# Performance work log

Hardware: AMD Instinct MI355X
Metric: run time of the kernel (lower is better)

## Reference

```python
import jax, jax.numpy as jnp
import numpy as np

N_NODES = 50000
N_EDGES = 800000
IN_FEATS = 32
OUT_FEATS = 32
NUM_HEADS = 4


def setup_inputs() -> dict:
    key = jax.random.key(0)
    ks = jax.random.split(key, 12)
    H, F, IN = NUM_HEADS, OUT_FEATS, IN_FEATS
    h = jax.random.normal(ks[0], (N_NODES, IN), dtype=jnp.float32)
    src = jax.random.randint(ks[1], (N_EDGES,), 0, N_NODES, dtype=jnp.int64)
    dst = jax.random.randint(ks[2], (N_EDGES,), 0, N_NODES, dtype=jnp.int64)
    s = 0.1
    W_gat = jax.random.normal(ks[3], (IN, H * F), dtype=jnp.float32) * s
    attn_l = jax.random.normal(ks[4], (H, F), dtype=jnp.float32) * s
    attn_r = jax.random.normal(ks[5], (H, F), dtype=jnp.float32) * s
    W_ih = jax.random.normal(ks[6], (3 * F, H * F), dtype=jnp.float32) * s
    W_hh = jax.random.normal(ks[7], (3 * F, F), dtype=jnp.float32) * s
    b_ih = jax.random.normal(ks[8], (3 * F,), dtype=jnp.float32) * s
    b_hh = jax.random.normal(ks[9], (3 * F,), dtype=jnp.float32) * s
    return {"h": h, "W_gat": W_gat, "attn_l": attn_l, "attn_r": attn_r,
            "W_ih": W_ih, "W_hh": W_hh, "b_ih": b_ih, "b_hh": b_hh,
            "src": src, "dst": dst}


def reference(h, W_gat, attn_l, attn_r, W_ih, W_hh, b_ih, b_hh, src, dst):
    N = h.shape[0]
    H, F = attn_l.shape
    # --- GATConv ---
    feat = (h @ W_gat).reshape(N, H, F)                      # (N,H,F)
    el = jnp.einsum('nhf,hf->nh', feat, attn_l)              # (N,H)
    er = jnp.einsum('nhf,hf->nh', feat, attn_r)              # (N,H)
    e = jax.nn.leaky_relu(el[src] + er[dst], 0.2)            # (E,H) edge logits
    emax = jax.ops.segment_max(e, dst, num_segments=N)       # per-dst max (stable)
    ee = jnp.exp(e - emax[dst])
    denom = jax.ops.segment_sum(ee, dst, num_segments=N)
    alpha = ee / denom[dst]                                  # segment softmax (E,H)
    msg = feat[src] * alpha[:, :, None]                      # (E,H,F)
    agg = jax.ops.segment_sum(msg, dst, num_segments=N)      # (N,H,F)
    x = agg.reshape(N, H * F)
    # --- GRUCell (torch semantics, gate order r,z,n) ---
    gi = x @ W_ih.T + b_ih                                   # (N,3F)
    gh = h @ W_hh.T + b_hh                                   # (N,3F)
    i_r, i_z, i_n = jnp.split(gi, 3, axis=1)
    h_r, h_z, h_n = jnp.split(gh, 3, axis=1)
    r = jax.nn.sigmoid(i_r + h_r)
    z = jax.nn.sigmoid(i_z + h_z)
    n = jnp.tanh(i_n + r * h_n)
    h_new = (1.0 - z) * n + z * h
    return jax.nn.elu(h_new)
```

## Files before the change

kernel.cpp:

```cpp
#include <hip/hip_runtime.h>
#include <hip/hip_bf16.h>
#include <cmath>

#define N_NODES 50000
#define N_EDGES 800000
#define CAP 64

#define NBINS 196
#define BIN_CAP 8192
#define CUR_PAD 32

#define P1_EPT 2
#define P1_EPB (1024 * P1_EPT)
#define P1_BLOCKS ((N_EDGES + P1_EPB - 1) / P1_EPB)

#define HB_BLOCKS 98
#define ELR_BLOCKS 196
#define WC_BLOCKS 30
#define NB_HB  (P1_BLOCKS)
#define NB_ELR (NB_HB + HB_BLOCKS)
#define NB_WC  (NB_ELR + ELR_BLOCKS)
#define NB_WGB (NB_WC + WC_BLOCKS)
#define PREP_TOTAL (NB_WGB + 1)

#define AGGR_BLOCKS (N_NODES / 16)

typedef __attribute__((ext_vector_type(8))) short bf16x8;
typedef __attribute__((ext_vector_type(4))) float f32x4;

__device__ inline short bfbits(float x) {
    __hip_bfloat16 t = __float2bfloat16(x);
    return *reinterpret_cast<short*>(&t);
}
__device__ inline unsigned short bfu16(float x) {
    __hip_bfloat16 t = __float2bfloat16(x);
    return *reinterpret_cast<unsigned short*>(&t);
}

__global__ __launch_bounds__(1024) void k_part_prep(
        const int* __restrict__ src, const int* __restrict__ dst,
        int* __restrict__ bin_cursor, unsigned* __restrict__ bin_buf,
        const float* __restrict__ h, const float* __restrict__ Wg,
        const float* __restrict__ al, const float* __restrict__ ar,
        const float* __restrict__ Wih, const float* __restrict__ Whh,
        unsigned short* __restrict__ hb, float* __restrict__ el,
        float* __restrict__ er, __hip_bfloat16* __restrict__ Wc,
        __hip_bfloat16* __restrict__ Wgb) {
    const int t = threadIdx.x;
    __shared__ union {
        struct {
            int bcnt[256], bofs[256], cur[256], gbase[256];
            int wt4[4];
            unsigned stage[P1_EPB];
        } part;
        __hip_bfloat16 vlr[16][32];
    } sm;

    if (blockIdx.x < P1_BLOCKS) {
        int* bcnt = sm.part.bcnt; int* bofs = sm.part.bofs;
        int* cur = sm.part.cur;   int* gbase = sm.part.gbase;
        int* wt4 = sm.part.wt4;   unsigned* stage = sm.part.stage;
        if (t < 256) bcnt[t] = 0;
        __syncthreads();
        int bn0 = -1, bn1 = -1;
        unsigned pk0 = 0, pk1 = 0;
        const int ebase = blockIdx.x * P1_EPB + t * 2;
        if (ebase < N_EDGES) {
            const int2 dd = *(const int2*)(dst + ebase);
            const int2 ss = *(const int2*)(src + ebase);
            bn0 = dd.x >> 8; pk0 = (unsigned)ss.x | ((unsigned)dd.x << 16);
            bn1 = dd.y >> 8; pk1 = (unsigned)ss.y | ((unsigned)dd.y << 16);
            atomicAdd(&bcnt[bn0], 1);
            atomicAdd(&bcnt[bn1], 1);
        }
        __syncthreads();
        int x = 0, vv = 0;
        if (t < 256) {
            vv = bcnt[t];
            x = vv;
            const int lane = t & 63;
#pragma unroll
            for (int m = 1; m < 64; m <<= 1) {
                const int y = __shfl_up(x, m, 64);
                if (lane >= m) x += y;
            }
            if (lane == 63) wt4[t >> 6] = x;
        }
        __syncthreads();
        if (t < 256) {
            const int wave4 = t >> 6;
            int wb = 0;
#pragma unroll
            for (int i = 0; i < 4; ++i) if (i < wave4) wb += wt4[i];
            const int off = wb + x - vv;
            bofs[t] = off;
            cur[t] = off;
            gbase[t] = (vv > 0) ? atomicAdd(&bin_cursor[t * CUR_PAD], vv) : 0;
        }
        __syncthreads();
        if (bn0 >= 0) {
            stage[atomicAdd(&cur[bn0], 1)] = pk0;
            stage[atomicAdd(&cur[bn1], 1)] = pk1;
        }
        __syncthreads();
        const int tot = wt4[0] + wt4[1] + wt4[2] + wt4[3];
        for (int i = t; i < tot; i += 1024) {
            const unsigned e = stage[i];
            const int b = e >> 24;
            const int gi = gbase[b] + (i - bofs[b]);
            if (gi < BIN_CAP) bin_buf[(size_t)b * BIN_CAP + gi] = e;
        }
        return;
    }
    if (blockIdx.x < NB_ELR) {
        const int idx = (blockIdx.x - NB_HB) * 1024 + t;
        const int base = idx * 16;
        if (base < N_NODES * 32) {
            const float4* hp = (const float4*)(h + base);
            const float4 v0 = hp[0], v1 = hp[1], v2 = hp[2], v3 = hp[3];
            unsigned o[8];
            o[0] = (unsigned)bfu16(v0.x) | ((unsigned)bfu16(v0.y) << 16);
            o[1] = (unsigned)bfu16(v0.z) | ((unsigned)bfu16(v0.w) << 16);
            o[2] = (unsigned)bfu16(v1.x) | ((unsigned)bfu16(v1.y) << 16);
            o[3] = (unsigned)bfu16(v1.z) | ((unsigned)bfu16(v1.w) << 16);
            o[4] = (unsigned)bfu16(v2.x) | ((unsigned)bfu16(v2.y) << 16);
            o[5] = (unsigned)bfu16(v2.z) | ((unsigned)bfu16(v2.w) << 16);
            o[6] = (unsigned)bfu16(v3.x) | ((unsigned)bfu16(v3.y) << 16);
            o[7] = (unsigned)bfu16(v3.z) | ((unsigned)bfu16(v3.w) << 16);
            uint4* op = (uint4*)(hb + base);
            op[0] = (uint4){o[0], o[1], o[2], o[3]};
            op[1] = (uint4){o[4], o[5], o[6], o[7]};
        }
        return;
    }
    if (blockIdx.x < NB_WC) {
        if (t < 512) {
            const int col = t >> 5, k = t & 31;
            float v = 0.f;
            if (col < 8) {
                const int hd = col & 3;
                const float* a = (col < 4) ? (al + hd * 32) : (ar + hd * 32);
                const float* w = Wg + k * 128 + hd * 32;
#pragma unroll
                for (int f = 0; f < 32; ++f) v = fmaf(w[f], a[f], v);
            }
            sm.vlr[col][k] = __float2bfloat16(v);
        }
        __syncthreads();
        const int wave = t >> 6, lane = t & 63;
        const int li = lane & 15, quad = lane >> 4;
        const int mt = (blockIdx.x - NB_ELR) * 16 + wave;
        if (mt >= AGGR_BLOCKS) return;
        const int m_base = mt * 16;
        bf16x8 a;
        {
            const float4* hp = (const float4*)(h + (size_t)(m_base + li) * 32 + quad * 8);
            const float4 f0 = hp[0], f1 = hp[1];
            a[0] = bfbits(f0.x); a[1] = bfbits(f0.y); a[2] = bfbits(f0.z); a[3] = bfbits(f0.w);
            a[4] = bfbits(f1.x); a[5] = bfbits(f1.y); a[6] = bfbits(f1.z); a[7] = bfbits(f1.w);
        }
        const bf16x8 b = *(const bf16x8*)(&sm.vlr[li][0] + quad * 8);
        f32x4 acc = (f32x4){0.f, 0.f, 0.f, 0.f};
        acc = __builtin_amdgcn_mfma_f32_16x16x32_bf16(a, b, acc, 0, 0, 0);
        if (li < 8) {
#pragma unroll
            for (int i = 0; i < 4; ++i) {
                const int m = m_base + quad * 4 + i;
                if (li < 4) el[m * 4 + li] = acc[i];
                else        er[m * 4 + (li - 4)] = acc[i];
            }
        }
        return;
    }
    if (blockIdx.x < NB_WGB) {
        const int idx = (blockIdx.x - NB_WC) * 1024 + t;
        const int r = idx / 160, k = idx - r * 160;
        float v = 0.f;
        if (r < 96) { if (k < 128) v = Wih[r * 128 + k]; }
        else        { if (k >= 128) v = Whh[(r - 96) * 32 + (k - 128)]; }
        Wc[idx] = __float2bfloat16(v);
        return;
    }
#pragma unroll
    for (int jj = 0; jj < 4; ++jj) {
        const int id = t * 4 + jj;
        const int k = id & 31, f = (id >> 5) & 31, hd = id >> 10;
        Wgb[id] = __float2bfloat16(Wg[k * 128 + hd * 32 + f]);
    }
}

__global__ __launch_bounds__(256) void k_aggr_gru(
        const int* __restrict__ bin_cursor, const unsigned* __restrict__ bin_buf,
        const unsigned char* __restrict__ hb,
        const float* __restrict__ el, const float* __restrict__ er,
        const float* __restrict__ h, const __hip_bfloat16* __restrict__ Wc,
        const __hip_bfloat16* __restrict__ Wgb,
        const float* __restrict__ bih, const float* __restrict__ bhh,
        float* __restrict__ out) {
    __shared__ unsigned short list[16][CAP];
    __shared__ int lcnt[16];
    __shared__ __hip_bfloat16 xh_tile[16][160];
    __shared__ float eel_s[4][256];
    __shared__ unsigned Sn[16][64];
    __shared__ float ex[2][3][16][16];
    const int t = threadIdx.x;
    const int wave = t >> 6;
    const int lane = t & 63;
    const int pb = blockIdx.x >> 4, six = blockIdx.x & 15;
    const int mbase = blockIdx.x * 16;

    if (t < 16) lcnt[t] = 0;
    __syncthreads();

    const int cbn = min(bin_cursor[pb * CUR_PAD], BIN_CAP);
    const uint4* bb4 = (const uint4*)(bin_buf + (size_t)pb * BIN_CAP);
    for (int i = t * 4; i < cbn; i += 1024) {
        const uint4 p4 = bb4[i >> 2];
#pragma unroll
        for (int k = 0; k < 4; ++k) {
            if (i + k < cbn) {
                const unsigned p = (&p4.x)[k];
                const int local = (p >> 16) & 255;
                if ((local >> 4) == six) {
                    const int dl = local & 15;
                    const int pos = atomicAdd(&lcnt[dl], 1);
                    if (pos < CAP) list[dl][pos] = (unsigned short)(p & 0xffff);
                }
            }
        }
    }
    __syncthreads();

    float* eel = eel_s[wave];
    const int hs = lane & 3;
    const int eq = lane >> 4;
    const int dw = lane & 15;
    for (int u = 0; u < 4; ++u) {
        const int row = wave * 4 + u;
        const int n = mbase + row;
        const float ern = er[n * 4 + hs];
        const int cnt = min(lcnt[row], CAP);
        const unsigned short* sl = list[row];
        eel[lane] = 0.f; eel[64 + lane] = 0.f;
        eel[128 + lane] = 0.f; eel[192 + lane] = 0.f;
        __builtin_amdgcn_wave_barrier();
        float psum = 0.f;
#pragma unroll
        for (int p = 0; p < 4; ++p) {
            const int j = p * 64 + lane;
            if (j < cnt * 4) {
                const int s = sl[j >> 2];
                float v = el[s * 4 + hs] + ern;
                v = v > 0.f ? v : 0.2f * v;
                const float e = __expf(v);
                eel[j] = e;
                psum += e;
            }
        }
        __builtin_amdgcn_wave_barrier();
        float a00 = 0.f, a01 = 0.f, a10 = 0.f, a11 = 0.f;
        float a20 = 0.f, a21 = 0.f, a30 = 0.f, a31 = 0.f;
        for (int i = 0; i < cnt; i += 16) {
            int e[4];
#pragma unroll
            for (int j = 0; j < 4; ++j) {
                const int ee = i + j * 4 + eq;
                e[j] = (ee < cnt) ? sl[ee] : 0;
            }
            unsigned q[4];
#pragma unroll
            for (int j = 0; j < 4; ++j)
                q[j] = *(const unsigned*)(hb + (size_t)e[j] * 64 + dw * 4);
#pragma unroll
            for (int j = 0; j < 4; ++j) {
                const int ee = i + j * 4 + eq;
                const float lo = __uint_as_float(q[j] << 16);
                const float hi = __uint_as_float(q[j] & 0xffff0000u);
                const float w0 = eel[ee * 4 + 0];
                const float w1 = eel[ee * 4 + 1];
                const float w2 = eel[ee * 4 + 2];
                const float w3 = eel[ee * 4 + 3];
                a00 = fmaf(w0, lo, a00); a01 = fmaf(w0, hi, a01);
                a10 = fmaf(w1, lo, a10); a11 = fmaf(w1, hi, a11);
                a20 = fmaf(w2, lo, a20); a21 = fmaf(w2, hi, a21);
                a30 = fmaf(w3, lo, a30); a31 = fmaf(w3, hi, a31);
            }
        }
        __builtin_amdgcn_wave_barrier();
#pragma unroll
        for (int m = 16; m < 64; m <<= 1) {
            a00 += __shfl_xor(a00, m, 64); a01 += __shfl_xor(a01, m, 64);
            a10 += __shfl_xor(a10, m, 64); a11 += __shfl_xor(a11, m, 64);
            a20 += __shfl_xor(a20, m, 64); a21 += __shfl_xor(a21, m, 64);
            a30 += __shfl_xor(a30, m, 64); a31 += __shfl_xor(a31, m, 64);
        }
#pragma unroll
        for (int m = 4; m < 64; m <<= 1) psum += __shfl_xor(psum, m, 64);
        const float inv0 = (cnt > 0) ? 1.f / __shfl(psum, 0, 64) : 0.f;
        const float inv1 = (cnt > 0) ? 1.f / __shfl(psum, 1, 64) : 0.f;
        const float inv2 = (cnt > 0) ? 1.f / __shfl(psum, 2, 64) : 0.f;
        const float inv3 = (cnt > 0) ? 1.f / __shfl(psum, 3, 64) : 0.f;
        if (lane < 16) {
            Sn[row][0 * 16 + lane] = (unsigned)bfu16(a00 * inv0) | ((unsigned)bfu16(a01 * inv0) << 16);
            Sn[row][1 * 16 + lane] = (unsigned)bfu16(a10 * inv1) | ((unsigned)bfu16(a11 * inv1) << 16);
            Sn[row][2 * 16 + lane] = (unsigned)bfu16(a20 * inv2) | ((unsigned)bfu16(a21 * inv2) << 16);
            Sn[row][3 * 16 + lane] = (unsigned)bfu16(a30 * inv3) | ((unsigned)bfu16(a31 * inv3) << 16);
        }
        if (lane < 32)
            xh_tile[row][128 + lane] = __float2bfloat16(h[(size_t)n * 32 + lane]);
    }
    __syncthreads();

    {
        const int li = lane & 15, quad = lane >> 4;
        const int head = wave;
        const __hip_bfloat16* snb = (const __hip_bfloat16*)&Sn[0][0];
        const bf16x8 aS = *(const bf16x8*)(snb + li * 128 + head * 32 + quad * 8);
        const bf16x8 b0 = *(const bf16x8*)(Wgb + (size_t)(head * 32 + li) * 32 + quad * 8);
        const bf16x8 b1 = *(const bf16x8*)(Wgb + (size_t)(head * 32 + 16 + li) * 32 + quad * 8);
        f32x4 c0 = (f32x4){0.f, 0.f, 0.f, 0.f};
        f32x4 c1 = (f32x4){0.f, 0.f, 0.f, 0.f};
        c0 = __builtin_amdgcn_mfma_f32_16x16x32_bf16(aS, b0, c0, 0, 0, 0);
        c1 = __builtin_amdgcn_mfma_f32_16x16x32_bf16(aS, b1, c1, 0, 0, 0);
#pragma unroll
        for (int i = 0; i < 4; ++i) {
            const int row = quad * 4 + i;
            xh_tile[row][head * 32 + li]      = __float2bfloat16(c0[i]);
            xh_tile[row][head * 32 + 16 + li] = __float2bfloat16(c1[i]);
        }
    }
    __syncthreads();

    const int li = lane & 15, quad = lane >> 4;
    const int cb = wave >> 1;
    const int ghrole = wave & 1;
    bf16x8 a[5];
#pragma unroll
    for (int s = 0; s < 5; ++s)
        a[s] = *(const bf16x8*)((const char*)&xh_tile[0][0] + li * 320 + s * 64 + quad * 16);
    f32x4 acc[3];
#pragma unroll
    for (int g = 0; g < 3; ++g) {
        acc[g] = (f32x4){0.f, 0.f, 0.f, 0.f};
        const int j = g * 2 + cb + ghrole * 6;
        const bf16x8* bp = (const bf16x8*)(Wc + (size_t)(j * 16 + li) * 160 + quad * 8);
        acc[g] = __builtin_amdgcn_mfma_f32_16x16x32_bf16(a[0], bp[0],  acc[g], 0, 0, 0);
        acc[g] = __builtin_amdgcn_mfma_f32_16x16x32_bf16(a[1], bp[4],  acc[g], 0, 0, 0);
        acc[g] = __builtin_amdgcn_mfma_f32_16x16x32_bf16(a[2], bp[8],  acc[g], 0, 0, 0);
        acc[g] = __builtin_amdgcn_mfma_f32_16x16x32_bf16(a[3], bp[12], acc[g], 0, 0, 0);
        acc[g] = __builtin_amdgcn_mfma_f32_16x16x32_bf16(a[4], bp[16], acc[g], 0, 0, 0);
    }
    if (ghrole) {
#pragma unroll
        for (int g = 0; g < 3; ++g)
#pragma unroll
            for (int i = 0; i < 4; ++i)
                ex[cb][g][quad * 4 + i][li] = acc[g][i];
    }
    __syncthreads();
    if (!ghrole) {
        const int c = cb * 16 + li;
        const float bir = bih[c],      bhr = bhh[c];
        const float biz = bih[32 + c], bhz = bhh[32 + c];
        const float bin = bih[64 + c], bhn = bhh[64 + c];
#pragma unroll
        for (int i = 0; i < 4; ++i) {
            const int row = quad * 4 + i;
            const int m = mbase + row;
            const float gr = acc[0][i] + bir + ex[cb][0][row][li] + bhr;
            const float gz = acc[1][i] + biz + ex[cb][1][row][li] + bhz;
            const float r = 1.f / (1.f + __expf(-gr));
            const float z = 1.f / (1.f + __expf(-gz));
            const float tv = acc[2][i] + bin + r * (ex[cb][2][row][li] + bhn);
            const float em = __expf(-2.f * fabsf(tv));
            const float nn = copysignf((1.f - em) / (1.f + em), tv);
            const float hv = h[(size_t)m * 32 + c];
            const float hn = (1.f - z) * nn + z * hv;
            out[(size_t)m * 32 + c] = hn > 0.f ? hn : (__expf(hn) - 1.f);
        }
    }
}

extern "C" void kernel_launch(void* const* d_in, const int* in_sizes, int n_in,
                              void* d_out, int out_size, void* d_ws, size_t ws_size,
                              hipStream_t stream) {
    const float* h   = (const float*)d_in[0];
    const float* Wg  = (const float*)d_in[1];
    const float* al  = (const float*)d_in[2];
    const float* ar  = (const float*)d_in[3];
    const float* Wih = (const float*)d_in[4];
    const float* Whh = (const float*)d_in[5];
    const float* bih = (const float*)d_in[6];
    const float* bhh = (const float*)d_in[7];
    const int* src   = (const int*)d_in[8];
    const int* dst   = (const int*)d_in[9];
    float* out = (float*)d_out;

    unsigned short* hb = (unsigned short*)d_ws;
    unsigned* bin_buf = (unsigned*)(hb + (size_t)N_NODES * 32);
    float* el = (float*)(bin_buf + (size_t)NBINS * BIN_CAP);
    float* er = el + (size_t)N_NODES * 4;
    __hip_bfloat16* Wc  = (__hip_bfloat16*)(er + (size_t)N_NODES * 4);
    __hip_bfloat16* Wgb = Wc + 30720;
    int* bin_cursor = (int*)(Wgb + 4096);

    hipMemsetAsync(bin_cursor, 0, NBINS * CUR_PAD * sizeof(int), stream);
    k_part_prep<<<PREP_TOTAL, 1024, 0, stream>>>(
        src, dst, bin_cursor, bin_buf, h, Wg, al, ar, Wih, Whh,
        hb, el, er, Wc, Wgb);
    k_aggr_gru<<<AGGR_BLOCKS, 256, 0, stream>>>(
        bin_cursor, bin_buf, (const unsigned char*)hb, el, er, h, Wc, Wgb,
        bih, bhh, out);
}
```

Before: 145.6 us.

## Replace binned edge partition with direct per-node adjacency slots via global atomics

Drops the two-level binning (block-local histogram, scan and staging, then per-block rescan of a 256-node bin) and has each edge atomically claim a slot in a fixed per-destination array of CAP source indices. The aggregation kernel then loads its 16 nodes' lists with one coalesced vector read instead of scanning a whole bin and filtering. Padding lanes now reuse the first source instead of node 0. This trades about 800k global atomics scattered over 50k counters, plus a 6.4MB padded slot array, for removing the bin scan in every aggregation block.

```diff
diff --git a/kernel.cpp b/kernel.cpp
--- a/kernel.cpp
+++ b/kernel.cpp
@@ -6,18 +6,14 @@
 #define N_EDGES 800000
 #define CAP 64
 
-#define NBINS 196
-#define BIN_CAP 8192
-#define CUR_PAD 32
-
-#define P1_EPT 2
-#define P1_EPB (1024 * P1_EPT)
-#define P1_BLOCKS ((N_EDGES + P1_EPB - 1) / P1_EPB)
+#define PART_EPT 4
+#define PART_EPB (1024 * PART_EPT)
+#define PART_BLOCKS ((N_EDGES + PART_EPB - 1) / PART_EPB)
 
 #define HB_BLOCKS 98
 #define ELR_BLOCKS 196
 #define WC_BLOCKS 30
-#define NB_HB  (P1_BLOCKS)
+#define NB_HB  (PART_BLOCKS)
 #define NB_ELR (NB_HB + HB_BLOCKS)
 #define NB_WC  (NB_ELR + ELR_BLOCKS)
 #define NB_WGB (NB_WC + WC_BLOCKS)
@@ -39,7 +35,7 @@
 
 __global__ __launch_bounds__(1024) void k_part_prep(
         const int* __restrict__ src, const int* __restrict__ dst,
-        int* __restrict__ bin_cursor, unsigned* __restrict__ bin_buf,
+        int* __restrict__ counts, unsigned short* __restrict__ srcs_p,
         const float* __restrict__ h, const float* __restrict__ Wg,
         const float* __restrict__ al, const float* __restrict__ ar,
         const float* __restrict__ Wih, const float* __restrict__ Whh,
@@ -47,68 +43,20 @@
         float* __restrict__ er, __hip_bfloat16* __restrict__ Wc,
         __hip_bfloat16* __restrict__ Wgb) {
     const int t = threadIdx.x;
-    __shared__ union {
-        struct {
-            int bcnt[256], bofs[256], cur[256], gbase[256];
-            int wt4[4];
-            unsigned stage[P1_EPB];
-        } part;
-        __hip_bfloat16 vlr[16][32];
-    } sm;
-
-    if (blockIdx.x < P1_BLOCKS) {
-        int* bcnt = sm.part.bcnt; int* bofs = sm.part.bofs;
-        int* cur = sm.part.cur;   int* gbase = sm.part.gbase;
-        int* wt4 = sm.part.wt4;   unsigned* stage = sm.part.stage;
-        if (t < 256) bcnt[t] = 0;
-        __syncthreads();
-        int bn0 = -1, bn1 = -1;
-        unsigned pk0 = 0, pk1 = 0;
-        const int ebase = blockIdx.x * P1_EPB + t * 2;
+    __shared__ __hip_bfloat16 vlr[16][32];
+
+    if (blockIdx.x < PART_BLOCKS) {
+        const int ebase = blockIdx.x * PART_EPB + t * PART_EPT;
         if (ebase < N_EDGES) {
-            const int2 dd = *(const int2*)(dst + ebase);
-            const int2 ss = *(const int2*)(src + ebase);
-            bn0 = dd.x >> 8; pk0 = (unsigned)ss.x | ((unsigned)dd.x << 16);
-            bn1 = dd.y >> 8; pk1 = (unsigned)ss.y | ((unsigned)dd.y << 16);
-            atomicAdd(&bcnt[bn0], 1);
-            atomicAdd(&bcnt[bn1], 1);
-        }
-        __syncthreads();
-        int x = 0, vv = 0;
-        if (t < 256) {
-            vv = bcnt[t];
-            x = vv;
-            const int lane = t & 63;
-#pragma unroll
-            for (int m = 1; m < 64; m <<= 1) {
-                const int y = __shfl_up(x, m, 64);
-                if (lane >= m) x += y;
-            }
-            if (lane == 63) wt4[t >> 6] = x;
-        }
-        __syncthreads();
-        if (t < 256) {
-            const int wave4 = t >> 6;
-            int wb = 0;
-#pragma unroll
-            for (int i = 0; i < 4; ++i) if (i < wave4) wb += wt4[i];
-            const int off = wb + x - vv;
-            bofs[t] = off;
-            cur[t] = off;
-            gbase[t] = (vv > 0) ? atomicAdd(&bin_cursor[t * CUR_PAD], vv) : 0;
-        }
-        __syncthreads();
-        if (bn0 >= 0) {
-            stage[atomicAdd(&cur[bn0], 1)] = pk0;
-            stage[atomicAdd(&cur[bn1], 1)] = pk1;
-        }
-        __syncthreads();
-        const int tot = wt4[0] + wt4[1] + wt4[2] + wt4[3];
-        for (int i = t; i < tot; i += 1024) {
-            const unsigned e = stage[i];
-            const int b = e >> 24;
-            const int gi = gbase[b] + (i - bofs[b]);
-            if (gi < BIN_CAP) bin_buf[(size_t)b * BIN_CAP + gi] = e;
+            const int4 dd = *(const int4*)(dst + ebase);
+            const int4 ss = *(const int4*)(src + ebase);
+#pragma unroll
+            for (int q = 0; q < PART_EPT; ++q) {
+                const int d = (&dd.x)[q];
+                const int s = (&ss.x)[q];
+                const int pos = atomicAdd(&counts[d], 1);
+                if (pos < CAP) srcs_p[(size_t)d * CAP + pos] = (unsigned short)s;
+            }
         }
         return;
     }
@@ -144,7 +92,7 @@
 #pragma unroll
                 for (int f = 0; f < 32; ++f) v = fmaf(w[f], a[f], v);
             }
-            sm.vlr[col][k] = __float2bfloat16(v);
+            vlr[col][k] = __float2bfloat16(v);
         }
         __syncthreads();
         const int wave = t >> 6, lane = t & 63;
@@ -159,7 +107,7 @@
             a[0] = bfbits(f0.x); a[1] = bfbits(f0.y); a[2] = bfbits(f0.z); a[3] = bfbits(f0.w);
             a[4] = bfbits(f1.x); a[5] = bfbits(f1.y); a[6] = bfbits(f1.z); a[7] = bfbits(f1.w);
         }
-        const bf16x8 b = *(const bf16x8*)(&sm.vlr[li][0] + quad * 8);
+        const bf16x8 b = *(const bf16x8*)(&vlr[li][0] + quad * 8);
         f32x4 acc = (f32x4){0.f, 0.f, 0.f, 0.f};
         acc = __builtin_amdgcn_mfma_f32_16x16x32_bf16(a, b, acc, 0, 0, 0);
         if (li < 8) {
@@ -190,8 +138,8 @@
 }
 
 __global__ __launch_bounds__(256) void k_aggr_gru(
-        const int* __restrict__ bin_cursor, const unsigned* __restrict__ bin_buf,
-        const unsigned char* __restrict__ hb,
+        const int* __restrict__ counts, const unsigned short* __restrict__ srcs_p,
+        const unsigned short* __restrict__ hb,
         const float* __restrict__ el, const float* __restrict__ er,
         const float* __restrict__ h, const __hip_bfloat16* __restrict__ Wc,
         const __hip_bfloat16* __restrict__ Wgb,
@@ -206,28 +154,12 @@
     const int t = threadIdx.x;
     const int wave = t >> 6;
     const int lane = t & 63;
-    const int pb = blockIdx.x >> 4, six = blockIdx.x & 15;
     const int mbase = blockIdx.x * 16;
 
-    if (t < 16) lcnt[t] = 0;
-    __syncthreads();
-
-    const int cbn = min(bin_cursor[pb * CUR_PAD], BIN_CAP);
-    const uint4* bb4 = (const uint4*)(bin_buf + (size_t)pb * BIN_CAP);
-    for (int i = t * 4; i < cbn; i += 1024) {
-        const uint4 p4 = bb4[i >> 2];
-#pragma unroll
-        for (int k = 0; k < 4; ++k) {
-            if (i + k < cbn) {
-                const unsigned p = (&p4.x)[k];
-                const int local = (p >> 16) & 255;
-                if ((local >> 4) == six) {
-                    const int dl = local & 15;
-                    const int pos = atomicAdd(&lcnt[dl], 1);
-                    if (pos < CAP) list[dl][pos] = (unsigned short)(p & 0xffff);
-                }
-            }
-        }
+    if (t < 16) lcnt[t] = min(counts[mbase + t], CAP);
+    {
+        const ushort4* sp = (const ushort4*)(srcs_p + (size_t)mbase * CAP);
+        ((ushort4*)&list[0][0])[t] = sp[t];
     }
     __syncthreads();
 
@@ -239,7 +171,7 @@
         const int row = wave * 4 + u;
         const int n = mbase + row;
         const float ern = er[n * 4 + hs];
-        const int cnt = min(lcnt[row], CAP);
+        const int cnt = lcnt[row];
         const unsigned short* sl = list[row];
         eel[lane] = 0.f; eel[64 + lane] = 0.f;
         eel[128 + lane] = 0.f; eel[192 + lane] = 0.f;
@@ -265,12 +197,12 @@
 #pragma unroll
             for (int j = 0; j < 4; ++j) {
                 const int ee = i + j * 4 + eq;
-                e[j] = (ee < cnt) ? sl[ee] : 0;
+                e[j] = (ee < cnt) ? sl[ee] : sl[0];
             }
             unsigned q[4];
 #pragma unroll
             for (int j = 0; j < 4; ++j)
-                q[j] = *(const unsigned*)(hb + (size_t)e[j] * 64 + dw * 4);
+                q[j] = *(const unsigned*)(hb + (size_t)e[j] * 32 + dw * 2);
 #pragma unroll
             for (int j = 0; j < 4; ++j) {
                 const int ee = i + j * 4 + eq;
@@ -397,18 +329,17 @@
     float* out = (float*)d_out;
 
     unsigned short* hb = (unsigned short*)d_ws;
-    unsigned* bin_buf = (unsigned*)(hb + (size_t)N_NODES * 32);
-    float* el = (float*)(bin_buf + (size_t)NBINS * BIN_CAP);
+    unsigned short* srcs_p = hb + (size_t)N_NODES * 32;
+    int* counts = (int*)(srcs_p + (size_t)N_NODES * CAP);
+    float* el = (float*)(counts + N_NODES);
     float* er = el + (size_t)N_NODES * 4;
     __hip_bfloat16* Wc  = (__hip_bfloat16*)(er + (size_t)N_NODES * 4);
     __hip_bfloat16* Wgb = Wc + 30720;
-    int* bin_cursor = (int*)(Wgb + 4096);
-
-    hipMemsetAsync(bin_cursor, 0, NBINS * CUR_PAD * sizeof(int), stream);
+
+    hipMemsetAsync(counts, 0, N_NODES * sizeof(int), stream);
     k_part_prep<<<PREP_TOTAL, 1024, 0, stream>>>(
-        src, dst, bin_cursor, bin_buf, h, Wg, al, ar, Wih, Whh,
+        src, dst, counts, srcs_p, h, Wg, al, ar, Wih, Whh,
         hb, el, er, Wc, Wgb);
     k_aggr_gru<<<AGGR_BLOCKS, 256, 0, stream>>>(
-        bin_cursor, bin_buf, (const unsigned char*)hb, el, er, h, Wc, Wgb,
-        bih, bhh, out);
-}
+        counts, srcs_p, hb, el, er, h, Wc, Wgb, bih, bhh, out);
+}
```

Result: slower. 164.4 us (+12.9%).
